# Kernel optimization log

Hardware: AMD Instinct MI355X
Metric: run time of the kernel (lower is better)

The kernel has to match this reference:

```python
import jax, jax.numpy as jnp
import numpy as np

B, S, H = 64, 1024, 1000

def setup_inputs() -> dict:
    key = jax.random.key(0)
    k1, k2, k3, k4 = jax.random.split(key, 4)
    h_tgt = jax.random.normal(k1, (B, 1, H), dtype=jnp.float32)
    h_src = jax.random.normal(k2, (B, S, H), dtype=jnp.float32)
    # nn.Linear(H, H) params: weight [H, H], bias [H]
    bound = 1.0 / np.sqrt(H)
    W = jax.random.uniform(k3, (H, H), dtype=jnp.float32, minval=-bound, maxval=bound)
    b = jax.random.uniform(k4, (H,), dtype=jnp.float32, minval=-bound, maxval=bound)
    return {"h_tgt": h_tgt, "h_src": h_src, "W": W, "b": b}

def reference(h_tgt, h_src, W, b):
    # score[b,t] = h_tgt[b,0] . (W @ h_src[b,t] + bias)  -- Luong general attention
    proj = jnp.einsum('bsh,gh->bsg', h_src, W) + b          # [B,S,H]
    score = jnp.einsum('bh,bsh->bs', h_tgt[:, 0], proj)      # [B,S]
    a = jax.nn.softmax(score, axis=1)                        # [B,S]
    c = jnp.einsum('bs,bsh->bh', a, h_src)[:, None, :]       # [B,1,H]
    return c
```

## Files before the change

### kernel.cpp

```cpp
#include <hip/hip_runtime.h>

constexpr int Bb = 64;
constexpr int Ss = 1024;
constexpr int Hh = 1000;
constexpr int CHUNKS = 64;
constexpr int CS = Ss / CHUNKS;
constexpr int BG = 4;
constexpr int GQ = 4;

__global__ __launch_bounds__(256) void proj_tgt_kernel(
    const float* __restrict__ h_tgt, const float* __restrict__ W,
    float* __restrict__ u)
{
    const int hl = threadIdx.x & 63;
    const int gq = threadIdx.x >> 6;
    const int h  = blockIdx.x * 64 + hl;
    const int b0 = blockIdx.y * BG;
    const bool hok = (h < Hh);

    float acc[BG] = {0.f, 0.f, 0.f, 0.f};
    const int g0 = gq * (Hh / GQ);
    const int g1 = g0 + (Hh / GQ);
    #pragma unroll 2
    for (int g = g0; g < g1; ++g) {
        const float w = hok ? W[g * Hh + h] : 0.f;
        #pragma unroll
        for (int bi = 0; bi < BG; ++bi)
            acc[bi] = fmaf(h_tgt[(b0 + bi) * Hh + g], w, acc[bi]);
    }

    __shared__ float red[GQ][BG][64];
    #pragma unroll
    for (int bi = 0; bi < BG; ++bi) red[gq][bi][hl] = acc[bi];
    __syncthreads();
    if (gq == 0 && hok) {
        #pragma unroll
        for (int bi = 0; bi < BG; ++bi) {
            const float s = red[0][bi][hl] + red[1][bi][hl]
                          + red[2][bi][hl] + red[3][bi][hl];
            u[(b0 + bi) * Hh + h] = s;
        }
    }
}

__global__ __launch_bounds__(256) void attn_partial_kernel(
    const float* __restrict__ h_src, const float* __restrict__ u,
    float* __restrict__ wsM, float* __restrict__ wsL, float* __restrict__ wsC)
{
    const int lane  = threadIdx.x & 63;
    const int wave  = (int)((blockIdx.x * blockDim.x + threadIdx.x) >> 6);
    const int b     = wave >> 6;
    const int chunk = wave & 63;
    const int s0    = chunk * CS;

    const float* ub = u + b * Hh;
    float4 uf[4];
    #pragma unroll
    for (int j = 0; j < 4; ++j) {
        const int d = j * 256 + lane * 4;
        uf[j] = (d < Hh) ? *(const float4*)(ub + d) : make_float4(0.f, 0.f, 0.f, 0.f);
    }

    float m = -INFINITY, l = 0.f;
    float4 c[4];
    #pragma unroll
    for (int j = 0; j < 4; ++j) c[j] = make_float4(0.f, 0.f, 0.f, 0.f);

    const float* xp = h_src + (size_t)(b * Ss + s0) * Hh;
    #pragma unroll 2
    for (int s = 0; s < CS; s += 2) {
        float4 x0[4], x1[4];
        #pragma unroll
        for (int j = 0; j < 4; ++j) {
            const int d = j * 256 + lane * 4;
            x0[j] = (d < Hh) ? *(const float4*)(xp + d)      : make_float4(0.f,0.f,0.f,0.f);
            x1[j] = (d < Hh) ? *(const float4*)(xp + Hh + d) : make_float4(0.f,0.f,0.f,0.f);
        }
        float p0 = 0.f, p1 = 0.f;
        #pragma unroll
        for (int j = 0; j < 4; ++j) {
            p0 = fmaf(x0[j].x, uf[j].x, p0); p0 = fmaf(x0[j].y, uf[j].y, p0);
            p0 = fmaf(x0[j].z, uf[j].z, p0); p0 = fmaf(x0[j].w, uf[j].w, p0);
            p1 = fmaf(x1[j].x, uf[j].x, p1); p1 = fmaf(x1[j].y, uf[j].y, p1);
            p1 = fmaf(x1[j].z, uf[j].z, p1); p1 = fmaf(x1[j].w, uf[j].w, p1);
        }
        #pragma unroll
        for (int off = 32; off > 0; off >>= 1) {
            p0 += __shfl_xor(p0, off, 64);
            p1 += __shfl_xor(p1, off, 64);
        }
        const float sc0 = p0, sc1 = p1;

        const float mn = fmaxf(m, fmaxf(sc0, sc1));
        if (mn > m) {
            const float scale = __expf(m - mn);
            m = mn;
            l *= scale;
            #pragma unroll
            for (int j = 0; j < 4; ++j) {
                c[j].x *= scale; c[j].y *= scale; c[j].z *= scale; c[j].w *= scale;
            }
        }
        const float e0 = __expf(sc0 - m);
        const float e1 = __expf(sc1 - m);
        l += e0 + e1;
        #pragma unroll
        for (int j = 0; j < 4; ++j) {
            c[j].x = fmaf(e0, x0[j].x, fmaf(e1, x1[j].x, c[j].x));
            c[j].y = fmaf(e0, x0[j].y, fmaf(e1, x1[j].y, c[j].y));
            c[j].z = fmaf(e0, x0[j].z, fmaf(e1, x1[j].z, c[j].z));
            c[j].w = fmaf(e0, x0[j].w, fmaf(e1, x1[j].w, c[j].w));
        }
        xp += 2 * Hh;
    }

    const int idx = b * CHUNKS + chunk;
    if (lane == 0) { wsM[idx] = m; wsL[idx] = l; }
    float* cw = wsC + (size_t)idx * Hh;
    #pragma unroll
    for (int j = 0; j < 4; ++j) {
        const int d = j * 256 + lane * 4;
        if (d < Hh) *(float4*)(cw + d) = c[j];
    }
}

__global__ __launch_bounds__(256) void combine_kernel(
    const float* __restrict__ wsM, const float* __restrict__ wsL,
    const float* __restrict__ wsC, float* __restrict__ out)
{
    const int b   = blockIdx.x;
    const int tid = (int)threadIdx.x;
    __shared__ float sw[CHUNKS];
    __shared__ float sInvL;

    if (tid < 64) {
        const float mi = wsM[b * CHUNKS + tid];
        const float li = wsL[b * CHUNKS + tid];
        float M = mi;
        #pragma unroll
        for (int off = 32; off > 0; off >>= 1) M = fmaxf(M, __shfl_xor(M, off, 64));
        const float w = __expf(mi - M);
        float L = w * li;
        #pragma unroll
        for (int off = 32; off > 0; off >>= 1) L += __shfl_xor(L, off, 64);
        sw[tid] = w;
        if (tid == 0) sInvL = 1.f / L;
    }
    __syncthreads();

    const int h = blockIdx.y * 250 + tid;
    if (tid < 250) {
        float acc = 0.f;
        #pragma unroll 8
        for (int i = 0; i < CHUNKS; ++i)
            acc = fmaf(sw[i], wsC[(size_t)(b * CHUNKS + i) * Hh + h], acc);
        out[b * Hh + h] = acc * sInvL;
    }
}

extern "C" void kernel_launch(void* const* d_in, const int* in_sizes, int n_in,
                              void* d_out, int out_size, void* d_ws, size_t ws_size,
                              hipStream_t stream) {
    const float* h_tgt = (const float*)d_in[0];
    const float* h_src = (const float*)d_in[1];
    const float* W     = (const float*)d_in[2];
    float* out = (float*)d_out;

    float* u   = (float*)d_ws;
    float* wsM = u + Bb * Hh;
    float* wsL = wsM + Bb * CHUNKS;
    float* wsC = wsL + Bb * CHUNKS;

    proj_tgt_kernel<<<dim3((Hh + 63) / 64, Bb / BG), 256, 0, stream>>>(h_tgt, W, u);
    attn_partial_kernel<<<(Bb * CHUNKS) / 4, 256, 0, stream>>>(h_src, u, wsM, wsL, wsC);
    combine_kernel<<<dim3(Bb, 4), 256, 0, stream>>>(wsM, wsL, wsC, out);
}
```

Measured before the change: 429.8 us.

## Split-K projection with vectorized W loads, separate reduce, nontemporal h_src loads

```diff
diff --git a/kernel.cpp b/kernel.cpp
--- a/kernel.cpp
+++ b/kernel.cpp
@@ -1,4 +1,6 @@
 #include <hip/hip_runtime.h>
+
+typedef float v4f __attribute__((ext_vector_type(4)));
 
 constexpr int Bb = 64;
 constexpr int Ss = 1024;
@@ -6,40 +8,53 @@
 constexpr int CHUNKS = 64;
 constexpr int CS = Ss / CHUNKS;
 constexpr int BG = 4;
-constexpr int GQ = 4;
+constexpr int GS = 8;
+constexpr int GL = Hh / GS;
 
-__global__ __launch_bounds__(256) void proj_tgt_kernel(
+__global__ __launch_bounds__(64) void proj_tgt_kernel(
     const float* __restrict__ h_tgt, const float* __restrict__ W,
-    float* __restrict__ u)
+    float* __restrict__ u_part)
 {
-    const int hl = threadIdx.x & 63;
-    const int gq = threadIdx.x >> 6;
-    const int h  = blockIdx.x * 64 + hl;
-    const int b0 = blockIdx.y * BG;
-    const bool hok = (h < Hh);
+    const int lane = (int)threadIdx.x;
+    const int b0   = (int)blockIdx.x * BG;
+    const int slot = (int)blockIdx.y * 64 + lane;
+    const int p    = (int)blockIdx.z;
+    const bool ok  = (slot < Hh / 4);
+    const int h    = slot * 4;
 
-    float acc[BG] = {0.f, 0.f, 0.f, 0.f};
-    const int g0 = gq * (Hh / GQ);
-    const int g1 = g0 + (Hh / GQ);
-    #pragma unroll 2
-    for (int g = g0; g < g1; ++g) {
-        const float w = hok ? W[g * Hh + h] : 0.f;
+    v4f acc[BG];
+    #pragma unroll
+    for (int bi = 0; bi < BG; ++bi) acc[bi] = (v4f){0.f, 0.f, 0.f, 0.f};
+
+    const float* wp = W + (size_t)(p * GL) * Hh + h;
+    const int gbase = p * GL;
+    #pragma unroll 4
+    for (int g = 0; g < GL; ++g) {
+        const v4f w4 = ok ? *(const v4f*)wp : (v4f){0.f, 0.f, 0.f, 0.f};
+        #pragma unroll
+        for (int bi = 0; bi < BG; ++bi) {
+            const float a = h_tgt[(b0 + bi) * Hh + gbase + g];
+            acc[bi] += a * w4;
+        }
+        wp += Hh;
+    }
+    if (ok) {
         #pragma unroll
         for (int bi = 0; bi < BG; ++bi)
-            acc[bi] = fmaf(h_tgt[(b0 + bi) * Hh + g], w, acc[bi]);
+            *(v4f*)(u_part + (size_t)(p * Bb + b0 + bi) * Hh + h) = acc[bi];
     }
+}
 
-    __shared__ float red[GQ][BG][64];
-    #pragma unroll
-    for (int bi = 0; bi < BG; ++bi) red[gq][bi][hl] = acc[bi];
-    __syncthreads();
-    if (gq == 0 && hok) {
+__global__ __launch_bounds__(256) void ureduce_kernel(
+    const float* __restrict__ u_part, float* __restrict__ u)
+{
+    const int i = (int)(blockIdx.x * blockDim.x + threadIdx.x);
+    if (i < Bb * Hh / 4) {
+        v4f s = (v4f){0.f, 0.f, 0.f, 0.f};
         #pragma unroll
-        for (int bi = 0; bi < BG; ++bi) {
-            const float s = red[0][bi][hl] + red[1][bi][hl]
-                          + red[2][bi][hl] + red[3][bi][hl];
-            u[(b0 + bi) * Hh + h] = s;
-        }
+        for (int p = 0; p < GS; ++p)
+            s += *(const v4f*)(u_part + (size_t)p * Bb * Hh + i * 4);
+        *(v4f*)(u + i * 4) = s;
     }
 }
 
@@ -54,27 +69,29 @@
     const int s0    = chunk * CS;
 
     const float* ub = u + b * Hh;
-    float4 uf[4];
+    v4f uf[4];
     #pragma unroll
     for (int j = 0; j < 4; ++j) {
         const int d = j * 256 + lane * 4;
-        uf[j] = (d < Hh) ? *(const float4*)(ub + d) : make_float4(0.f, 0.f, 0.f, 0.f);
+        uf[j] = (d < Hh) ? *(const v4f*)(ub + d) : (v4f){0.f, 0.f, 0.f, 0.f};
     }
 
     float m = -INFINITY, l = 0.f;
-    float4 c[4];
+    v4f c[4];
     #pragma unroll
-    for (int j = 0; j < 4; ++j) c[j] = make_float4(0.f, 0.f, 0.f, 0.f);
+    for (int j = 0; j < 4; ++j) c[j] = (v4f){0.f, 0.f, 0.f, 0.f};
 
     const float* xp = h_src + (size_t)(b * Ss + s0) * Hh;
     #pragma unroll 2
     for (int s = 0; s < CS; s += 2) {
-        float4 x0[4], x1[4];
+        v4f x0[4], x1[4];
         #pragma unroll
         for (int j = 0; j < 4; ++j) {
             const int d = j * 256 + lane * 4;
-            x0[j] = (d < Hh) ? *(const float4*)(xp + d)      : make_float4(0.f,0.f,0.f,0.f);
-            x1[j] = (d < Hh) ? *(const float4*)(xp + Hh + d) : make_float4(0.f,0.f,0.f,0.f);
+            x0[j] = (d < Hh) ? __builtin_nontemporal_load((const v4f*)(xp + d))
+                             : (v4f){0.f, 0.f, 0.f, 0.f};
+            x1[j] = (d < Hh) ? __builtin_nontemporal_load((const v4f*)(xp + Hh + d))
+                             : (v4f){0.f, 0.f, 0.f, 0.f};
         }
         float p0 = 0.f, p1 = 0.f;
         #pragma unroll
@@ -97,9 +114,7 @@
             m = mn;
             l *= scale;
             #pragma unroll
-            for (int j = 0; j < 4; ++j) {
-                c[j].x *= scale; c[j].y *= scale; c[j].z *= scale; c[j].w *= scale;
-            }
+            for (int j = 0; j < 4; ++j) c[j] *= scale;
         }
         const float e0 = __expf(sc0 - m);
         const float e1 = __expf(sc1 - m);
@@ -120,7 +135,7 @@
     #pragma unroll
     for (int j = 0; j < 4; ++j) {
         const int d = j * 256 + lane * 4;
-        if (d < Hh) *(float4*)(cw + d) = c[j];
+        if (d < Hh) *(v4f*)(cw + d) = c[j];
     }
 }
 
@@ -166,12 +181,14 @@
     const float* W     = (const float*)d_in[2];
     float* out = (float*)d_out;
 
-    float* u   = (float*)d_ws;
-    float* wsM = u + Bb * Hh;
-    float* wsL = wsM + Bb * CHUNKS;
-    float* wsC = wsL + Bb * CHUNKS;
+    float* u      = (float*)d_ws;
+    float* wsM    = u + Bb * Hh;
+    float* wsL    = wsM + Bb * CHUNKS;
+    float* wsC    = wsL + Bb * CHUNKS;
+    float* u_part = wsC + (size_t)Bb * CHUNKS * Hh;
 
-    proj_tgt_kernel<<<dim3((Hh + 63) / 64, Bb / BG), 256, 0, stream>>>(h_tgt, W, u);
+    proj_tgt_kernel<<<dim3(Bb / BG, 4, GS), 64, 0, stream>>>(h_tgt, W, u_part);
+    ureduce_kernel<<<(Bb * Hh / 4 + 255) / 256, 256, 0, stream>>>(u_part, u);
     attn_partial_kernel<<<(Bb * CHUNKS) / 4, 256, 0, stream>>>(h_src, u, wsM, wsL, wsC);
     combine_kernel<<<dim3(Bb, 4), 256, 0, stream>>>(wsM, wsL, wsC, out);
 }
```

Result: faster. 383.0 us (-10.9%).
